# Optimization experiments

Hardware: AMD Instinct MI355X
Metric: run time of the kernel (lower is better)

## Reference

```python
import jax, jax.numpy as jnp
import numpy as np

NUM_NODES = 100000
NUM_EDGES = 640000
D_IN = 128
D_OUT = 128


def setup_inputs() -> dict:
    key = jax.random.key(0)
    k_x, k_s, k_t, k_w, k_lin = jax.random.split(key, 5)
    x = jax.random.normal(k_x, (NUM_NODES, D_IN), dtype=jnp.float32)
    source = jax.random.randint(k_s, (NUM_EDGES,), 0, NUM_NODES, dtype=jnp.int32)
    target = jax.random.randint(k_t, (NUM_EDGES,), 0, NUM_NODES, dtype=jnp.int32)
    edge_weights = jax.random.uniform(k_w, (NUM_EDGES,), dtype=jnp.float32)
    # nn.Linear weight, shape (out, in), kaiming-uniform-ish init
    bound = 1.0 / np.sqrt(D_IN)
    W = jax.random.uniform(k_lin, (D_OUT, D_IN), dtype=jnp.float32, minval=-bound, maxval=bound)
    return {"x": x, "W": W, "edge_weights": edge_weights, "source": source, "target": target}


def reference(x, W, edge_weights, source, target):
    # LinearMessageCreator: project all nodes first (as in the torch code), then gather per edge
    h = jnp.einsum("nd,od->no", x, W)            # (num_nodes, d_out)
    msg = h[source] * edge_weights[:, None]       # (num_edges, d_out)
    # SumAggregator: scatter-add messages into target nodes
    delta = jax.ops.segment_sum(msg, target, num_segments=x.shape[0])
    # OnlyUpdate: return aggregated messages
    return delta
```

## Files before the change

kernel.cpp:

```cpp
#include <hip/hip_runtime.h>
#include <hip/hip_bf16.h>

#define NN 100000
#define NE 640000
#define D 128

#define SCAN_CHUNK 1024
#define NBLK ((NN + SCAN_CHUNK - 1) / SCAN_CHUNK)

#define OFF_COUNTS  0u
#define OFF_OFFSETS 400000u
#define OFF_CURSOR  800016u
#define OFF_BSUM    1200016u
#define OFF_BSUMEX  1200528u
#define OFF_PE      1201040u
#define WS_T2       6321040u
#define OFF_XB      6321040u
#define WS_FULL     31921040u

typedef __attribute__((ext_vector_type(8))) short bf16x8;
typedef __attribute__((ext_vector_type(4))) float f32x4;

__device__ __forceinline__ float bflo(unsigned u) { return __uint_as_float(u << 16); }
__device__ __forceinline__ float bfhi(unsigned u) { return __uint_as_float(u & 0xffff0000u); }
__device__ __forceinline__ unsigned bfpk(float x, float y) {
    __hip_bfloat16 bx = __float2bfloat16(x), by = __float2bfloat16(y);
    return (unsigned)(*(unsigned short*)&bx) | ((unsigned)(*(unsigned short*)&by) << 16);
}

__global__ __launch_bounds__(256) void k_hist(const int* __restrict__ tgt,
                                              int* __restrict__ counts) {
    int e = blockIdx.x * 256 + threadIdx.x;
    if (e < NE) atomicAdd(&counts[tgt[e]], 1);
}

__global__ __launch_bounds__(256) void k_scan_part(const int* __restrict__ counts,
                                                   int* __restrict__ bsum) {
    __shared__ int sd[256];
    int b = blockIdx.x, t = threadIdx.x;
    int base = b * SCAN_CHUNK + t * 4;
    int s = 0;
    #pragma unroll
    for (int k = 0; k < 4; ++k) { int i = base + k; s += (i < NN) ? counts[i] : 0; }
    sd[t] = s; __syncthreads();
    for (int off = 128; off > 0; off >>= 1) {
        if (t < off) sd[t] += sd[t + off];
        __syncthreads();
    }
    if (t == 0) bsum[b] = sd[0];
}

__global__ __launch_bounds__(128) void k_scan_mid(const int* __restrict__ bsum,
                                                  int* __restrict__ bsumex,
                                                  int* __restrict__ offsets) {
    __shared__ int sd[128];
    int t = threadIdx.x;
    int v = (t < NBLK) ? bsum[t] : 0;
    sd[t] = v; __syncthreads();
    for (int off = 1; off < 128; off <<= 1) {
        int tmp = (t >= off) ? sd[t - off] : 0;
        __syncthreads();
        sd[t] += tmp;
        __syncthreads();
    }
    if (t < NBLK) bsumex[t] = sd[t] - v;
    if (t == 0) offsets[NN] = NE;
}

__global__ __launch_bounds__(256) void k_scan_final(const int* __restrict__ counts,
                                                    const int* __restrict__ bsumex,
                                                    int* __restrict__ offsets,
                                                    int* __restrict__ cursor) {
    __shared__ int sd[256];
    int b = blockIdx.x, t = threadIdx.x;
    int base = b * SCAN_CHUNK + t * 4;
    int c[4]; int s = 0;
    #pragma unroll
    for (int k = 0; k < 4; ++k) { int i = base + k; c[k] = (i < NN) ? counts[i] : 0; s += c[k]; }
    sd[t] = s; __syncthreads();
    for (int off = 1; off < 256; off <<= 1) {
        int tmp = (t >= off) ? sd[t - off] : 0;
        __syncthreads();
        sd[t] += tmp;
        __syncthreads();
    }
    int run = sd[t] - s + bsumex[b];
    #pragma unroll
    for (int k = 0; k < 4; ++k) {
        int i = base + k;
        if (i < NN) { offsets[i] = run; cursor[i] = run; }
        run += c[k];
    }
}

#define FILL_BLKS ((NE + 255) / 256)
#define CONV_BLKS ((NN * 64 + 255) / 256)

__global__ __launch_bounds__(256) void k_fill_conv(const int* __restrict__ src,
                                                   const int* __restrict__ tgt,
                                                   const float* __restrict__ ew,
                                                   int* __restrict__ cursor,
                                                   int2* __restrict__ pe,
                                                   const float* __restrict__ x,
                                                   unsigned* __restrict__ xb) {
    int b = blockIdx.x;
    if (b < FILL_BLKS) {
        int e = b * 256 + threadIdx.x;
        if (e < NE) {
            int t = tgt[e];
            int p = atomicAdd(&cursor[t], 1);
            pe[p] = make_int2(src[e], __float_as_int(ew[e]));
        }
    } else {
        int i = (b - FILL_BLKS) * 256 + threadIdx.x;
        if (i < NN * 64) {
            float2 v = ((const float2*)x)[i];
            xb[i] = bfpk(v.x, v.y);
        }
    }
}

__global__ __launch_bounds__(256) void k_fill(const int* __restrict__ src,
                                              const int* __restrict__ tgt,
                                              const float* __restrict__ ew,
                                              int* __restrict__ cursor,
                                              int2* __restrict__ pe) {
    int e = blockIdx.x * 256 + threadIdx.x;
    if (e < NE) {
        int t = tgt[e];
        int p = atomicAdd(&cursor[t], 1);
        pe[p] = make_int2(src[e], __float_as_int(ew[e]));
    }
}

#define KP 136

__global__ __launch_bounds__(512) void k_gather_project(const unsigned* __restrict__ xb,
                                                        const int* __restrict__ offsets,
                                                        const int2* __restrict__ pe,
                                                        const float* __restrict__ W,
                                                        float* __restrict__ out) {
    __shared__ __align__(16) unsigned short Wb[D][KP];
    __shared__ __align__(16) unsigned short As[64][KP];

    const int tid = threadIdx.x;
    const long nb = (long)blockIdx.x * 64;

    const float4* W4 = (const float4*)W;
    #pragma unroll
    for (int it = 0; it < 8; ++it) {
        int idx = it * 512 + tid;
        int f = idx >> 5, kq = idx & 31;
        float4 v = W4[idx];
        *(uint2*)&Wb[f][kq * 4] = make_uint2(bfpk(v.x, v.y), bfpk(v.z, v.w));
    }

    const int w = tid >> 6;
    const int lane = tid & 63;

    for (int j = 0; j < 8; ++j) {
        int n = w * 8 + j;
        long node = nb + n;
        int beg = 0, end = 0;
        if (node < NN) { beg = offsets[node]; end = offsets[node + 1]; }
        float a0 = 0.f, a1 = 0.f;
        int2 e = (beg < end) ? pe[beg] : make_int2(0, 0);
        for (int i = beg; i < end; ++i) {
            int2 en = (i + 1 < end) ? pe[i + 1] : make_int2(0, 0);
            unsigned v = xb[(size_t)e.x * 64 + lane];
            float wt = __int_as_float(e.y);
            a0 = fmaf(bflo(v), wt, a0);
            a1 = fmaf(bfhi(v), wt, a1);
            e = en;
        }
        *(unsigned*)&As[n][lane * 2] = bfpk(a0, a1);
    }
    __syncthreads();

    const int lr = lane & 15;
    const int lg = lane >> 4;
    const int r0 = (w >> 1) * 16;
    const int ct0 = (w & 1) * 4;

    bf16x8 afrag[4];
    #pragma unroll
    for (int ks = 0; ks < 4; ++ks)
        afrag[ks] = *(const bf16x8*)&As[r0 + lr][ks * 32 + lg * 8];

    #pragma unroll
    for (int c = 0; c < 4; ++c) {
        int ct = ct0 + c;
        f32x4 acc = {0.f, 0.f, 0.f, 0.f};
        #pragma unroll
        for (int ks = 0; ks < 4; ++ks) {
            bf16x8 bfrag = *(const bf16x8*)&Wb[ct * 16 + lr][ks * 32 + lg * 8];
            acc = __builtin_amdgcn_mfma_f32_16x16x32_bf16(afrag[ks], bfrag, acc, 0, 0, 0);
        }
        #pragma unroll
        for (int r = 0; r < 4; ++r) {
            long gn = nb + r0 + lg * 4 + r;
            if (gn < NN) out[gn * D + ct * 16 + lr] = acc[r];
        }
    }
}

__global__ __launch_bounds__(256) void k_gather_f32(const float* __restrict__ x,
                                                    const int* __restrict__ offsets,
                                                    const int2* __restrict__ pe,
                                                    float* __restrict__ out) {
    int wid = blockIdx.x * 4 + (threadIdx.x >> 6);
    int lane = threadIdx.x & 63;
    if (wid >= NN) return;
    int beg = offsets[wid], end = offsets[wid + 1];
    const float2* x2 = (const float2*)x;
    float a0 = 0.f, a1 = 0.f;
    int2 e = (beg < end) ? pe[beg] : make_int2(0, 0);
    for (int i = beg; i < end; ++i) {
        int2 en = (i + 1 < end) ? pe[i + 1] : make_int2(0, 0);
        float2 v = x2[(size_t)e.x * 64 + lane];
        float w = __int_as_float(e.y);
        a0 = fmaf(v.x, w, a0);
        a1 = fmaf(v.y, w, a1);
        e = en;
    }
    ((float2*)out)[(size_t)wid * 64 + lane] = make_float2(a0, a1);
}

__global__ __launch_bounds__(256) void k_project_mfma(const float* __restrict__ W,
                                                      float* __restrict__ io) {
    __shared__ __align__(16) unsigned short Wb[D][KP];
    __shared__ __align__(16) unsigned short As[64][KP];

    const int tid = threadIdx.x;
    const long nb = (long)blockIdx.x * 64;

    const float4* W4 = (const float4*)W;
    #pragma unroll
    for (int it = 0; it < 16; ++it) {
        int idx = it * 256 + tid;
        int f = idx >> 5, kq = idx & 31;
        float4 v = W4[idx];
        *(uint2*)&Wb[f][kq * 4] = make_uint2(bfpk(v.x, v.y), bfpk(v.z, v.w));
    }
    const float4* io4 = (const float4*)io;
    #pragma unroll
    for (int it = 0; it < 8; ++it) {
        int idx = it * 256 + tid;
        int n = idx >> 5, kq = idx & 31;
        long node = nb + n;
        float4 v = (node < NN) ? io4[node * 32 + kq]
                               : make_float4(0.f, 0.f, 0.f, 0.f);
        *(uint2*)&As[n][kq * 4] = make_uint2(bfpk(v.x, v.y), bfpk(v.z, v.w));
    }
    __syncthreads();

    const int w  = tid >> 6;
    const int l  = tid & 63;
    const int lr = l & 15;
    const int lg = l >> 4;
    const int r0 = w * 16;

    bf16x8 afrag[4];
    #pragma unroll
    for (int ks = 0; ks < 4; ++ks)
        afrag[ks] = *(const bf16x8*)&As[r0 + lr][ks * 32 + lg * 8];

    #pragma unroll
    for (int ct = 0; ct < 8; ++ct) {
        f32x4 acc = {0.f, 0.f, 0.f, 0.f};
        #pragma unroll
        for (int ks = 0; ks < 4; ++ks) {
            bf16x8 bfrag = *(const bf16x8*)&Wb[ct * 16 + lr][ks * 32 + lg * 8];
            acc = __builtin_amdgcn_mfma_f32_16x16x32_bf16(afrag[ks], bfrag, acc, 0, 0, 0);
        }
        #pragma unroll
        for (int r = 0; r < 4; ++r) {
            long gn = nb + r0 + lg * 4 + r;
            if (gn < NN) io[gn * D + ct * 16 + lr] = acc[r];
        }
    }
}

__global__ __launch_bounds__(256) void gcn_scatter(const float* __restrict__ x,
                                                   const float* __restrict__ ew,
                                                   const int* __restrict__ src,
                                                   const int* __restrict__ tgt,
                                                   float* __restrict__ out) {
    int tid = blockIdx.x * 256 + threadIdx.x;
    int e = tid >> 5;
    int t = tid & 31;
    if (e >= NE) return;
    int s = src[e];
    int g = tgt[e];
    float w = ew[e];
    float4 xv = reinterpret_cast<const float4*>(x)[s * 32 + t];
    float* dst = out + (size_t)g * D + (t << 2);
    atomicAdd(dst + 0, xv.x * w);
    atomicAdd(dst + 1, xv.y * w);
    atomicAdd(dst + 2, xv.z * w);
    atomicAdd(dst + 3, xv.w * w);
}

extern "C" void kernel_launch(void* const* d_in, const int* in_sizes, int n_in,
                              void* d_out, int out_size, void* d_ws, size_t ws_size,
                              hipStream_t stream) {
    const float* x   = (const float*)d_in[0];
    const float* W   = (const float*)d_in[1];
    const float* ew  = (const float*)d_in[2];
    const int*   src = (const int*)d_in[3];
    const int*   tgt = (const int*)d_in[4];
    float* out = (float*)d_out;

    if (ws_size >= WS_T2) {
        char* ws = (char*)d_ws;
        int*  counts  = (int*)(ws + OFF_COUNTS);
        int*  offsets = (int*)(ws + OFF_OFFSETS);
        int*  cursor  = (int*)(ws + OFF_CURSOR);
        int*  bsum    = (int*)(ws + OFF_BSUM);
        int*  bsumex  = (int*)(ws + OFF_BSUMEX);
        int2* pe      = (int2*)(ws + OFF_PE);

        hipMemsetAsync(counts, 0, (size_t)NN * sizeof(int), stream);
        k_hist<<<(NE + 255) / 256, 256, 0, stream>>>(tgt, counts);
        k_scan_part<<<NBLK, 256, 0, stream>>>(counts, bsum);
        k_scan_mid<<<1, 128, 0, stream>>>(bsum, bsumex, offsets);
        k_scan_final<<<NBLK, 256, 0, stream>>>(counts, bsumex, offsets, cursor);

        if (ws_size >= WS_FULL) {
            unsigned* xb = (unsigned*)(ws + OFF_XB);
            k_fill_conv<<<FILL_BLKS + CONV_BLKS, 256, 0, stream>>>(src, tgt, ew, cursor, pe, x, xb);
            k_gather_project<<<(NN + 63) / 64, 512, 0, stream>>>(xb, offsets, pe, W, out);
        } else {
            k_fill<<<FILL_BLKS, 256, 0, stream>>>(src, tgt, ew, cursor, pe);
            k_gather_f32<<<(NN + 3) / 4, 256, 0, stream>>>(x, offsets, pe, out);
            k_project_mfma<<<(NN + 63) / 64, 256, 0, stream>>>(W, out);
        }
    } else {
        hipMemsetAsync(out, 0, (size_t)out_size * sizeof(float), stream);
        gcn_scatter<<<(NE * 32 + 255) / 256, 256, 0, stream>>>(x, ew, src, tgt, out);
        k_project_mfma<<<(NN + 63) / 64, 256, 0, stream>>>(W, out);
    }
}
```

Before: 264.8 us.

## Fold scan-mid into scan-final and precompute bf16 W in fill kernel

Removes the single-block middle scan launch: each final-scan block now reduces the preceding block sums itself to get its base offset. W's fp32-to-bf16 conversion moves into extra blocks of the fill/convert kernel, writing into the counts region (reused after the scan). The gather-project kernel then reads W fragments straight from global memory instead of staging them in LDS, which cuts LDS use and per-block conversion work. The cost is redundant block-sum reductions and uncached global loads of W fragments inside the MFMA loop.

```diff
diff --git a/kernel.cpp b/kernel.cpp
--- a/kernel.cpp
+++ b/kernel.cpp
@@ -9,6 +9,7 @@
 #define NBLK ((NN + SCAN_CHUNK - 1) / SCAN_CHUNK)
 
 #define OFF_COUNTS  0u
+#define OFF_WBF     0u
 #define OFF_OFFSETS 400000u
 #define OFF_CURSOR  800016u
 #define OFF_BSUM    1200016u
@@ -50,29 +51,22 @@
     if (t == 0) bsum[b] = sd[0];
 }
 
-__global__ __launch_bounds__(128) void k_scan_mid(const int* __restrict__ bsum,
-                                                  int* __restrict__ bsumex,
-                                                  int* __restrict__ offsets) {
-    __shared__ int sd[128];
-    int t = threadIdx.x;
-    int v = (t < NBLK) ? bsum[t] : 0;
-    sd[t] = v; __syncthreads();
-    for (int off = 1; off < 128; off <<= 1) {
-        int tmp = (t >= off) ? sd[t - off] : 0;
-        __syncthreads();
-        sd[t] += tmp;
-        __syncthreads();
-    }
-    if (t < NBLK) bsumex[t] = sd[t] - v;
-    if (t == 0) offsets[NN] = NE;
-}
-
 __global__ __launch_bounds__(256) void k_scan_final(const int* __restrict__ counts,
-                                                    const int* __restrict__ bsumex,
+                                                    const int* __restrict__ bsum,
                                                     int* __restrict__ offsets,
                                                     int* __restrict__ cursor) {
     __shared__ int sd[256];
     int b = blockIdx.x, t = threadIdx.x;
+
+    sd[t] = (t < b) ? bsum[t] : 0;
+    __syncthreads();
+    for (int off = 128; off > 0; off >>= 1) {
+        if (t < off) sd[t] += sd[t + off];
+        __syncthreads();
+    }
+    int base_b = sd[0];
+    __syncthreads();
+
     int base = b * SCAN_CHUNK + t * 4;
     int c[4]; int s = 0;
     #pragma unroll
@@ -84,17 +78,19 @@
         sd[t] += tmp;
         __syncthreads();
     }
-    int run = sd[t] - s + bsumex[b];
+    int run = sd[t] - s + base_b;
     #pragma unroll
     for (int k = 0; k < 4; ++k) {
         int i = base + k;
         if (i < NN) { offsets[i] = run; cursor[i] = run; }
         run += c[k];
     }
+    if (b == 0 && t == 0) offsets[NN] = NE;
 }
 
 #define FILL_BLKS ((NE + 255) / 256)
 #define CONV_BLKS ((NN * 64 + 255) / 256)
+#define WBF_BLKS  16
 
 __global__ __launch_bounds__(256) void k_fill_conv(const int* __restrict__ src,
                                                    const int* __restrict__ tgt,
@@ -102,7 +98,9 @@
                                                    int* __restrict__ cursor,
                                                    int2* __restrict__ pe,
                                                    const float* __restrict__ x,
-                                                   unsigned* __restrict__ xb) {
+                                                   unsigned* __restrict__ xb,
+                                                   const float* __restrict__ W,
+                                                   unsigned* __restrict__ wbf) {
     int b = blockIdx.x;
     if (b < FILL_BLKS) {
         int e = b * 256 + threadIdx.x;
@@ -111,12 +109,17 @@
             int p = atomicAdd(&cursor[t], 1);
             pe[p] = make_int2(src[e], __float_as_int(ew[e]));
         }
-    } else {
+    } else if (b < FILL_BLKS + CONV_BLKS) {
         int i = (b - FILL_BLKS) * 256 + threadIdx.x;
         if (i < NN * 64) {
             float2 v = ((const float2*)x)[i];
             xb[i] = bfpk(v.x, v.y);
         }
+    } else {
+        int idx = (b - FILL_BLKS - CONV_BLKS) * 256 + threadIdx.x;
+        int f = idx >> 5, kq = idx & 31;
+        float4 v = ((const float4*)W)[idx];
+        *(uint2*)&wbf[f * 64 + kq * 2] = make_uint2(bfpk(v.x, v.y), bfpk(v.z, v.w));
     }
 }
 
@@ -138,22 +141,12 @@
 __global__ __launch_bounds__(512) void k_gather_project(const unsigned* __restrict__ xb,
                                                         const int* __restrict__ offsets,
                                                         const int2* __restrict__ pe,
-                                                        const float* __restrict__ W,
+                                                        const unsigned short* __restrict__ wbf,
                                                         float* __restrict__ out) {
-    __shared__ __align__(16) unsigned short Wb[D][KP];
     __shared__ __align__(16) unsigned short As[64][KP];
 
     const int tid = threadIdx.x;
     const long nb = (long)blockIdx.x * 64;
-
-    const float4* W4 = (const float4*)W;
-    #pragma unroll
-    for (int it = 0; it < 8; ++it) {
-        int idx = it * 512 + tid;
-        int f = idx >> 5, kq = idx & 31;
-        float4 v = W4[idx];
-        *(uint2*)&Wb[f][kq * 4] = make_uint2(bfpk(v.x, v.y), bfpk(v.z, v.w));
-    }
 
     const int w = tid >> 6;
     const int lane = tid & 63;
@@ -193,7 +186,7 @@
         f32x4 acc = {0.f, 0.f, 0.f, 0.f};
         #pragma unroll
         for (int ks = 0; ks < 4; ++ks) {
-            bf16x8 bfrag = *(const bf16x8*)&Wb[ct * 16 + lr][ks * 32 + lg * 8];
+            bf16x8 bfrag = *(const bf16x8*)&wbf[(ct * 16 + lr) * 128 + ks * 32 + lg * 8];
             acc = __builtin_amdgcn_mfma_f32_16x16x32_bf16(afrag[ks], bfrag, acc, 0, 0, 0);
         }
         #pragma unroll
@@ -317,19 +310,20 @@
         int*  offsets = (int*)(ws + OFF_OFFSETS);
         int*  cursor  = (int*)(ws + OFF_CURSOR);
         int*  bsum    = (int*)(ws + OFF_BSUM);
-        int*  bsumex  = (int*)(ws + OFF_BSUMEX);
         int2* pe      = (int2*)(ws + OFF_PE);
 
         hipMemsetAsync(counts, 0, (size_t)NN * sizeof(int), stream);
         k_hist<<<(NE + 255) / 256, 256, 0, stream>>>(tgt, counts);
         k_scan_part<<<NBLK, 256, 0, stream>>>(counts, bsum);
-        k_scan_mid<<<1, 128, 0, stream>>>(bsum, bsumex, offsets);
-        k_scan_final<<<NBLK, 256, 0, stream>>>(counts, bsumex, offsets, cursor);
+        k_scan_final<<<NBLK, 256, 0, stream>>>(counts, bsum, offsets, cursor);
 
         if (ws_size >= WS_FULL) {
-            unsigned* xb = (unsigned*)(ws + OFF_XB);
-            k_fill_conv<<<FILL_BLKS + CONV_BLKS, 256, 0, stream>>>(src, tgt, ew, cursor, pe, x, xb);
-            k_gather_project<<<(NN + 63) / 64, 512, 0, stream>>>(xb, offsets, pe, W, out);
+            unsigned* xb  = (unsigned*)(ws + OFF_XB);
+            unsigned* wbf = (unsigned*)(ws + OFF_WBF);
+            k_fill_conv<<<FILL_BLKS + CONV_BLKS + WBF_BLKS, 256, 0, stream>>>(
+                src, tgt, ew, cursor, pe, x, xb, W, wbf);
+            k_gather_project<<<(NN + 63) / 64, 512, 0, stream>>>(
+                xb, offsets, pe, (const unsigned short*)wbf, out);
         } else {
             k_fill<<<FILL_BLKS, 256, 0, stream>>>(src, tgt, ew, cursor, pe);
             k_gather_f32<<<(NN + 3) / 4, 256, 0, stream>>>(x, offsets, pe, out);
```

Measured after the change: 255.6 us. 1.04x faster.
